# Kernel optimization log

Measured on AMD Instinct MI355X. Metric: run time of the kernel, lower is better.

Reference implementation:

```python
import jax, jax.numpy as jnp
import numpy as np
from jax import lax

V, E, H, B, S = 50257, 512, 1024, 128, 256

def setup_inputs() -> dict:
    key = jax.random.key(0)
    k0, k1, k2, k3, k4, k5 = jax.random.split(key, 6)
    scale = 1.0 / np.sqrt(H)  # PyTorch LSTMCell init range ~ U(-1/sqrt(H), 1/sqrt(H))
    return {
        "inputs": jax.random.randint(k0, (B, S), 0, V),
        "embed_table": jax.random.normal(k1, (V, E), dtype=jnp.float32) * 0.02,
        "W_ih": jax.random.uniform(k2, (4 * H, E), dtype=jnp.float32, minval=-scale, maxval=scale),
        "W_hh": jax.random.uniform(k3, (4 * H, H), dtype=jnp.float32, minval=-scale, maxval=scale),
        "b_ih": jax.random.uniform(k4, (4 * H,), dtype=jnp.float32, minval=-scale, maxval=scale),
        "b_hh": jax.random.uniform(k5, (4 * H,), dtype=jnp.float32, minval=-scale, maxval=scale),
    }

def reference(inputs, embed_table, W_ih, W_hh, b_ih, b_hh):
    # Embedding lookup: [B, S, E]
    embeds = embed_table[inputs]
    bias = b_ih + b_hh  # [4H]

    def step(h, x_t):
        # x_t: [B, E], h: [B, H]
        gates = x_t @ W_ih.T + h @ W_hh.T + bias  # [B, 4H]
        i, f, g, o = jnp.split(gates, 4, axis=-1)  # PyTorch gate order: i, f, g, o
        # FAITHFUL to original bug: new cell state is discarded each step, so the
        # carried cell state is always zero -> c_t = sigmoid(i) * tanh(g).
        c_t = jax.nn.sigmoid(i) * jnp.tanh(g)
        h_new = jax.nn.sigmoid(o) * jnp.tanh(c_t)
        return h_new, None

    h0 = jnp.zeros((B, H), dtype=embeds.dtype)
    xs = jnp.swapaxes(embeds, 0, 1)  # [S, B, E]
    h_last, _ = lax.scan(step, h0, xs)
    return h_last  # [B, H]
```

## Files before the change

kernel.cpp:

```cpp
#include <hip/hip_runtime.h>
#include <hip/hip_fp16.h>


typedef __fp16 f16x8 __attribute__((ext_vector_type(8)));
typedef __fp16 f16x4 __attribute__((ext_vector_type(4)));
typedef float  f32x4 __attribute__((ext_vector_type(4)));

#define MFMA16(a, b, c) __builtin_amdgcn_mfma_f32_16x16x32_f16(a, b, c, 0, 0, 0)

__device__ __forceinline__ float sigmoid_f(float x) {
  return 1.f / (1.f + __expf(-x));
}
__device__ __forceinline__ float tanh_f(float x) {
  x = fminf(fmaxf(x, -15.f), 15.f);
  float e = __expf(2.f * x);
  return (e - 1.f) / (e + 1.f);
}

static constexpr int SS = 256;

__global__ void prep_kernel(const float* __restrict__ W_ih, const float* __restrict__ W_hh,
                            const float* __restrict__ b_ih, const float* __restrict__ b_hh,
                            __fp16* __restrict__ Wi3, __fp16* __restrict__ Wh3,
                            float* __restrict__ bias3) {
  int j3 = blockIdx.x;
  int g = j3 >> 10, j = j3 & 1023;
  int orig = (g == 0 ? 0 : (g == 1 ? 2048 : 3072)) + j;
  int tid = threadIdx.x;
  {
    float4 v = *(const float4*)(W_hh + (size_t)orig * 1024 + tid * 4);
    f16x4 o = {(__fp16)v.x, (__fp16)v.y, (__fp16)v.z, (__fp16)v.w};
    *(f16x4*)(Wh3 + (size_t)j3 * 1024 + tid * 4) = o;
  }
  if (tid < 128) {
    float4 v = *(const float4*)(W_ih + (size_t)orig * 512 + tid * 4);
    f16x4 o = {(__fp16)v.x, (__fp16)v.y, (__fp16)v.z, (__fp16)v.w};
    *(f16x4*)(Wi3 + (size_t)j3 * 512 + tid * 4) = o;
  }
  if (tid == 0) bias3[j3] = b_ih[orig] + b_hh[orig];
}

__global__ void gather_kernel(const int* __restrict__ tok, const float* __restrict__ emb,
                              __fp16* __restrict__ X) {
  int m = blockIdx.x;
  int t = m >> 7, b = m & 127;
  int tk = tok[b * SS + t];
  int e0 = threadIdx.x * 8;
  const float* src = emb + (size_t)tk * 512 + e0;
  float4 v0 = *(const float4*)src;
  float4 v1 = *(const float4*)(src + 4);
  f16x8 o;
  o[0] = (__fp16)v0.x; o[1] = (__fp16)v0.y; o[2] = (__fp16)v0.z; o[3] = (__fp16)v0.w;
  o[4] = (__fp16)v1.x; o[5] = (__fp16)v1.y; o[6] = (__fp16)v1.z; o[7] = (__fp16)v1.w;
  *(f16x8*)(X + (size_t)m * 512 + e0) = o;
}

__global__ __launch_bounds__(512, 2) void recur_kernel(const __fp16* __restrict__ Wh3,
                                                       const __fp16* __restrict__ Wi3,
                                                       const __fp16* __restrict__ X,
                                                       const float* __restrict__ bias3,
                                                       __fp16* __restrict__ hbuf,
                                                       int* __restrict__ cnt,
                                                       float* __restrict__ out) {
  const int bid = blockIdx.x;
  const int bg = bid & 7, n = bid >> 3;
  const int b0 = bg * 16, j0 = n * 32;
  const int tid = threadIdx.x, wid = tid >> 6, lane = tid & 63;
  const int l15 = lane & 15, quad = lane >> 4;
  const int kq = wid >> 1, ct = wid & 1;
  const int ct_e = wid & 1, rq = wid >> 1;
  const int lr = lane >> 4;

  __shared__ float gbuf[2][4][3][2][16][20];

  f16x8 wh[3][8];
  f16x8 wi[3][4];
#pragma unroll
  for (int g = 0; g < 3; ++g) {
    const __fp16* wr = Wh3 + (size_t)(g * 1024 + j0 + ct * 16 + l15) * 1024 + kq * 256 + quad * 8;
#pragma unroll
    for (int kk = 0; kk < 8; ++kk) wh[g][kk] = *(const f16x8*)(wr + kk * 32);
    const __fp16* wr2 = Wi3 + (size_t)(g * 1024 + j0 + ct * 16 + l15) * 512 + kq * 128 + quad * 8;
#pragma unroll
    for (int kk = 0; kk < 4; ++kk) wi[g][kk] = *(const f16x8*)(wr2 + kk * 32);
  }

  float bs[3];
#pragma unroll
  for (int g = 0; g < 3; ++g) bs[g] = bias3[g * 1024 + j0 + ct_e * 16 + l15];

  const __fp16* xrow = X + (size_t)(b0 + l15) * 512 + kq * 128 + quad * 8;
  const __fp16* hrow = hbuf + (size_t)(b0 + l15) * 1024 + kq * 256 + quad * 8;
  int* cbase = cnt + bg * (SS * 16);

  f16x8 xa[4];
#pragma unroll
  for (int kk = 0; kk < 4; ++kk) xa[kk] = *(const f16x8*)(xrow + kk * 32);

  for (int t = 0; t < SS; ++t) {
    f32x4 acc[3];
#pragma unroll
    for (int g = 0; g < 3; ++g) {
      f32x4 z = {0.f, 0.f, 0.f, 0.f};
      acc[g] = z;
    }
#pragma unroll
    for (int kk = 0; kk < 4; ++kk)
#pragma unroll
      for (int g = 0; g < 3; ++g)
        acc[g] = MFMA16(xa[kk], wi[g][kk], acc[g]);
    {
      const int tn = (t + 1 < SS) ? t + 1 : t;
      const __fp16* xp = xrow + (size_t)tn * 65536;
#pragma unroll
      for (int kk = 0; kk < 4; ++kk) xa[kk] = *(const f16x8*)(xp + kk * 32);
    }
    if (t > 0) {
      const int* pollp = cbase + t * 16;
      for (;;) {
        int v = __hip_atomic_load(pollp, __ATOMIC_RELAXED, __HIP_MEMORY_SCOPE_AGENT);
        if (v >= 32) break;
        __builtin_amdgcn_s_sleep(1);
      }
      asm volatile("" ::: "memory");
    }
    f16x8 ha[8];
    {
      const __fp16* hp = hrow + (size_t)t * 131072;
#pragma unroll
      for (int kk = 0; kk < 8; ++kk) ha[kk] = *(const f16x8*)(hp + kk * 32);
    }
#pragma unroll
    for (int kk = 0; kk < 8; ++kk)
#pragma unroll
      for (int g = 0; g < 3; ++g)
        acc[g] = MFMA16(ha[kk], wh[g][kk], acc[g]);
    const int tp = t & 1;
#pragma unroll
    for (int g = 0; g < 3; ++g)
#pragma unroll
      for (int r = 0; r < 4; ++r)
        gbuf[tp][kq][g][ct][quad * 4 + r][l15] = acc[g][r];
    __syncthreads();
    {
      const int row_i = rq * 4 + lr;
      float s[3];
#pragma unroll
      for (int g = 0; g < 3; ++g)
        s[g] = gbuf[tp][0][g][ct_e][row_i][l15] + gbuf[tp][1][g][ct_e][row_i][l15] +
               gbuf[tp][2][g][ct_e][row_i][l15] + gbuf[tp][3][g][ct_e][row_i][l15];
      float gi = s[0] + bs[0];
      float gg = s[1] + bs[1];
      float go = s[2] + bs[2];
      float cv = sigmoid_f(gi) * tanh_f(gg);
      float hN = sigmoid_f(go) * tanh_f(cv);
      const int row = b0 + row_i;
      const int col = j0 + ct_e * 16 + l15;
      if (t == SS - 1) out[(size_t)row * 1024 + col] = hN;
      else hbuf[(size_t)(t + 1) * 131072 + (size_t)row * 1024 + col] = (__fp16)hN;
    }
    if (t < SS - 1) {
      asm volatile("s_waitcnt vmcnt(0)" ::: "memory");
      __syncthreads();
      if (tid == 0)
        __hip_atomic_fetch_add(cbase + (t + 1) * 16, 1,
                               __ATOMIC_RELAXED, __HIP_MEMORY_SCOPE_AGENT);
    }
  }
}

extern "C" void kernel_launch(void* const* d_in, const int* in_sizes, int n_in,
                              void* d_out, int out_size, void* d_ws, size_t ws_size,
                              hipStream_t stream) {
  const int*   tok  = (const int*)d_in[0];
  const float* emb  = (const float*)d_in[1];
  const float* W_ih = (const float*)d_in[2];
  const float* W_hh = (const float*)d_in[3];
  const float* b_ih = (const float*)d_in[4];
  const float* b_hh = (const float*)d_in[5];
  float* out = (float*)d_out;
  char* ws = (char*)d_ws;

  __fp16* X     = (__fp16*)(ws + 0);
  __fp16* Wi3   = (__fp16*)(ws + 33554432);
  __fp16* Wh3   = (__fp16*)(ws + 36700160);
  float*  bias3 = (float*) (ws + 42991616);
  int*    cnt   = (int*)   (ws + 43003904);
  __fp16* hbuf  = (__fp16*)(ws + 43134976);

  (void)hipMemsetAsync(cnt, 0, 131072, stream);
  (void)hipMemsetAsync(hbuf, 0, 131072 * 2, stream);

  prep_kernel<<<3072, 256, 0, stream>>>(W_ih, W_hh, b_ih, b_hh, Wi3, Wh3, bias3);
  gather_kernel<<<32768, 64, 0, stream>>>(tok, emb, X);
  recur_kernel<<<256, 512, 0, stream>>>(Wh3, Wi3, X, bias3, hbuf, cnt, out);
}
```

Baseline: 1.235 ms.

## Halve per-block column tile, launch 512 four-wave blocks, relax step barrier fencing

Each block now owns 16 hidden columns instead of 32 and runs 4 waves, so the grid grows to 512 blocks and the per-step arrival counter must reach 64. Each wave still holds its K-quarter of the weights in registers, and inline asm pins those weight registers. The explicit vmcnt wait and memory clobber around the step flag are removed. Instead, the h loads take a fake address dependency on the polled counter value (v>>8), which keeps them ordered after the poll. The intent is more parallelism and less per-step synchronisation latency. In exchange there are twice as many blocks signalling each counter, and the weaker ordering of hbuf stores before the release add risks memory-visibility races.

```diff
diff --git a/kernel.cpp b/kernel.cpp
--- a/kernel.cpp
+++ b/kernel.cpp
@@ -55,7 +55,7 @@
   *(f16x8*)(X + (size_t)m * 512 + e0) = o;
 }
 
-__global__ __launch_bounds__(512, 2) void recur_kernel(const __fp16* __restrict__ Wh3,
+__global__ __launch_bounds__(256, 2) void recur_kernel(const __fp16* __restrict__ Wh3,
                                                        const __fp16* __restrict__ Wi3,
                                                        const __fp16* __restrict__ X,
                                                        const float* __restrict__ bias3,
@@ -64,30 +64,35 @@
                                                        float* __restrict__ out) {
   const int bid = blockIdx.x;
   const int bg = bid & 7, n = bid >> 3;
-  const int b0 = bg * 16, j0 = n * 32;
+  const int b0 = bg * 16, j0 = n * 16;
   const int tid = threadIdx.x, wid = tid >> 6, lane = tid & 63;
   const int l15 = lane & 15, quad = lane >> 4;
-  const int kq = wid >> 1, ct = wid & 1;
-  const int ct_e = wid & 1, rq = wid >> 1;
-  const int lr = lane >> 4;
-
-  __shared__ float gbuf[2][4][3][2][16][20];
+  const int kq = wid;
+
+  __shared__ float gbuf[2][4][3][16][20];
 
   f16x8 wh[3][8];
   f16x8 wi[3][4];
 #pragma unroll
   for (int g = 0; g < 3; ++g) {
-    const __fp16* wr = Wh3 + (size_t)(g * 1024 + j0 + ct * 16 + l15) * 1024 + kq * 256 + quad * 8;
+    const __fp16* wr = Wh3 + (size_t)(g * 1024 + j0 + l15) * 1024 + kq * 256 + quad * 8;
 #pragma unroll
     for (int kk = 0; kk < 8; ++kk) wh[g][kk] = *(const f16x8*)(wr + kk * 32);
-    const __fp16* wr2 = Wi3 + (size_t)(g * 1024 + j0 + ct * 16 + l15) * 512 + kq * 128 + quad * 8;
+    const __fp16* wr2 = Wi3 + (size_t)(g * 1024 + j0 + l15) * 512 + kq * 128 + quad * 8;
 #pragma unroll
     for (int kk = 0; kk < 4; ++kk) wi[g][kk] = *(const f16x8*)(wr2 + kk * 32);
   }
+#pragma unroll
+  for (int g = 0; g < 3; ++g) {
+#pragma unroll
+    for (int kk = 0; kk < 8; ++kk) asm volatile("" : "+v"(wh[g][kk]));
+#pragma unroll
+    for (int kk = 0; kk < 4; ++kk) asm volatile("" : "+v"(wi[g][kk]));
+  }
 
   float bs[3];
 #pragma unroll
-  for (int g = 0; g < 3; ++g) bs[g] = bias3[g * 1024 + j0 + ct_e * 16 + l15];
+  for (int g = 0; g < 3; ++g) bs[g] = bias3[g * 1024 + j0 + l15];
 
   const __fp16* xrow = X + (size_t)(b0 + l15) * 512 + kq * 128 + quad * 8;
   const __fp16* hrow = hbuf + (size_t)(b0 + l15) * 1024 + kq * 256 + quad * 8;
@@ -115,18 +120,18 @@
 #pragma unroll
       for (int kk = 0; kk < 4; ++kk) xa[kk] = *(const f16x8*)(xp + kk * 32);
     }
+    int v = 64;
     if (t > 0) {
       const int* pollp = cbase + t * 16;
       for (;;) {
-        int v = __hip_atomic_load(pollp, __ATOMIC_RELAXED, __HIP_MEMORY_SCOPE_AGENT);
-        if (v >= 32) break;
+        v = __hip_atomic_load(pollp, __ATOMIC_RELAXED, __HIP_MEMORY_SCOPE_AGENT);
+        if (v >= 64) break;
         __builtin_amdgcn_s_sleep(1);
       }
-      asm volatile("" ::: "memory");
     }
     f16x8 ha[8];
     {
-      const __fp16* hp = hrow + (size_t)t * 131072;
+      const __fp16* hp = hrow + (size_t)t * 131072 + (v >> 8);
 #pragma unroll
       for (int kk = 0; kk < 8; ++kk) ha[kk] = *(const f16x8*)(hp + kk * 32);
     }
@@ -140,27 +145,26 @@
     for (int g = 0; g < 3; ++g)
 #pragma unroll
       for (int r = 0; r < 4; ++r)
-        gbuf[tp][kq][g][ct][quad * 4 + r][l15] = acc[g][r];
+        gbuf[tp][kq][g][quad * 4 + r][l15] = acc[g][r];
     __syncthreads();
     {
-      const int row_i = rq * 4 + lr;
+      const int row_i = kq * 4 + quad;
       float s[3];
 #pragma unroll
       for (int g = 0; g < 3; ++g)
-        s[g] = gbuf[tp][0][g][ct_e][row_i][l15] + gbuf[tp][1][g][ct_e][row_i][l15] +
-               gbuf[tp][2][g][ct_e][row_i][l15] + gbuf[tp][3][g][ct_e][row_i][l15];
+        s[g] = gbuf[tp][0][g][row_i][l15] + gbuf[tp][1][g][row_i][l15] +
+               gbuf[tp][2][g][row_i][l15] + gbuf[tp][3][g][row_i][l15];
       float gi = s[0] + bs[0];
       float gg = s[1] + bs[1];
       float go = s[2] + bs[2];
       float cv = sigmoid_f(gi) * tanh_f(gg);
       float hN = sigmoid_f(go) * tanh_f(cv);
       const int row = b0 + row_i;
-      const int col = j0 + ct_e * 16 + l15;
+      const int col = j0 + l15;
       if (t == SS - 1) out[(size_t)row * 1024 + col] = hN;
       else hbuf[(size_t)(t + 1) * 131072 + (size_t)row * 1024 + col] = (__fp16)hN;
     }
     if (t < SS - 1) {
-      asm volatile("s_waitcnt vmcnt(0)" ::: "memory");
       __syncthreads();
       if (tid == 0)
         __hip_atomic_fetch_add(cbase + (t + 1) * 16, 1,
@@ -193,5 +197,5 @@
 
   prep_kernel<<<3072, 256, 0, stream>>>(W_ih, W_hh, b_ih, b_hh, Wi3, Wh3, bias3);
   gather_kernel<<<32768, 64, 0, stream>>>(tok, emb, X);
-  recur_kernel<<<256, 512, 0, stream>>>(Wh3, Wi3, X, bias3, hbuf, cnt, out);
-}
+  recur_kernel<<<512, 256, 0, stream>>>(Wh3, Wi3, X, bias3, hbuf, cnt, out);
+}
```

New measurement: 2.109 ms. 1.71x slower.

## Halve recurrent block to 4 waves with 2-way K split and per-wave signaling

Applied to the files above, without the earlier changes.

Changes the recurrent kernel from 8 waves with a 4-way K split to 4 waves with a 2-way K split. Each wave now holds twice as many weight registers. The cross-wave reduction becomes a single LDS handoff from half the waves, and the post-step __syncthreads is removed in favour of per-wave atomic increments, with the poll threshold raised to 64. The aim is to shorten the per-timestep critical path by cutting LDS reduction and barrier work. The cost is much higher register pressure (wh[3][16] plus ha[16] per lane), more serial MFMA per wave, and more atomic traffic. Sigmoid and tanh also switch to a hardware reciprocal instead of division.

```diff
diff --git a/kernel.cpp b/kernel.cpp
--- a/kernel.cpp
+++ b/kernel.cpp
@@ -8,13 +8,14 @@
 
 #define MFMA16(a, b, c) __builtin_amdgcn_mfma_f32_16x16x32_f16(a, b, c, 0, 0, 0)
 
+__device__ __forceinline__ float rcp_f(float x) { return __builtin_amdgcn_rcpf(x); }
 __device__ __forceinline__ float sigmoid_f(float x) {
-  return 1.f / (1.f + __expf(-x));
+  return rcp_f(1.f + __expf(-x));
 }
 __device__ __forceinline__ float tanh_f(float x) {
   x = fminf(fmaxf(x, -15.f), 15.f);
   float e = __expf(2.f * x);
-  return (e - 1.f) / (e + 1.f);
+  return 1.f - 2.f * rcp_f(e + 1.f);
 }
 
 static constexpr int SS = 256;
@@ -55,7 +56,7 @@
   *(f16x8*)(X + (size_t)m * 512 + e0) = o;
 }
 
-__global__ __launch_bounds__(512, 2) void recur_kernel(const __fp16* __restrict__ Wh3,
+__global__ __launch_bounds__(256, 1) void recur_kernel(const __fp16* __restrict__ Wh3,
                                                        const __fp16* __restrict__ Wi3,
                                                        const __fp16* __restrict__ X,
                                                        const float* __restrict__ bias3,
@@ -67,35 +68,34 @@
   const int b0 = bg * 16, j0 = n * 32;
   const int tid = threadIdx.x, wid = tid >> 6, lane = tid & 63;
   const int l15 = lane & 15, quad = lane >> 4;
-  const int kq = wid >> 1, ct = wid & 1;
-  const int ct_e = wid & 1, rq = wid >> 1;
-  const int lr = lane >> 4;
+  const int tile = wid & 1, kh = wid >> 1;
+  const int col = j0 + tile * 16 + l15;
 
-  __shared__ float gbuf[2][4][3][2][16][20];
+  __shared__ float gbuf[2][2][3][16][20];
 
-  f16x8 wh[3][8];
-  f16x8 wi[3][4];
+  f16x8 wi[3][8];
+  f16x8 wh[3][16];
 #pragma unroll
   for (int g = 0; g < 3; ++g) {
-    const __fp16* wr = Wh3 + (size_t)(g * 1024 + j0 + ct * 16 + l15) * 1024 + kq * 256 + quad * 8;
+    const __fp16* wr2 = Wi3 + (size_t)(g * 1024 + col) * 512 + kh * 256 + quad * 8;
 #pragma unroll
-    for (int kk = 0; kk < 8; ++kk) wh[g][kk] = *(const f16x8*)(wr + kk * 32);
-    const __fp16* wr2 = Wi3 + (size_t)(g * 1024 + j0 + ct * 16 + l15) * 512 + kq * 128 + quad * 8;
+    for (int kk = 0; kk < 8; ++kk) wi[g][kk] = *(const f16x8*)(wr2 + kk * 32);
+    const __fp16* wr = Wh3 + (size_t)(g * 1024 + col) * 1024 + kh * 512 + quad * 8;
 #pragma unroll
-    for (int kk = 0; kk < 4; ++kk) wi[g][kk] = *(const f16x8*)(wr2 + kk * 32);
+    for (int kk = 0; kk < 16; ++kk) wh[g][kk] = *(const f16x8*)(wr + kk * 32);
   }
 
   float bs[3];
 #pragma unroll
-  for (int g = 0; g < 3; ++g) bs[g] = bias3[g * 1024 + j0 + ct_e * 16 + l15];
+  for (int g = 0; g < 3; ++g) bs[g] = bias3[g * 1024 + col];
 
-  const __fp16* xrow = X + (size_t)(b0 + l15) * 512 + kq * 128 + quad * 8;
-  const __fp16* hrow = hbuf + (size_t)(b0 + l15) * 1024 + kq * 256 + quad * 8;
+  const __fp16* xrow = X + (size_t)(b0 + l15) * 512 + kh * 256 + quad * 8;
+  const __fp16* hrow = hbuf + (size_t)(b0 + l15) * 1024 + kh * 512 + quad * 8;
   int* cbase = cnt + bg * (SS * 16);
 
-  f16x8 xa[4];
+  f16x8 xa[8];
 #pragma unroll
-  for (int kk = 0; kk < 4; ++kk) xa[kk] = *(const f16x8*)(xrow + kk * 32);
+  for (int kk = 0; kk < 8; ++kk) xa[kk] = *(const f16x8*)(xrow + kk * 32);
 
   for (int t = 0; t < SS; ++t) {
     f32x4 acc[3];
@@ -105,7 +105,7 @@
       acc[g] = z;
     }
 #pragma unroll
-    for (int kk = 0; kk < 4; ++kk)
+    for (int kk = 0; kk < 8; ++kk)
 #pragma unroll
       for (int g = 0; g < 3; ++g)
         acc[g] = MFMA16(xa[kk], wi[g][kk], acc[g]);
@@ -113,58 +113,56 @@
       const int tn = (t + 1 < SS) ? t + 1 : t;
       const __fp16* xp = xrow + (size_t)tn * 65536;
 #pragma unroll
-      for (int kk = 0; kk < 4; ++kk) xa[kk] = *(const f16x8*)(xp + kk * 32);
+      for (int kk = 0; kk < 8; ++kk) xa[kk] = *(const f16x8*)(xp + kk * 32);
     }
     if (t > 0) {
       const int* pollp = cbase + t * 16;
       for (;;) {
         int v = __hip_atomic_load(pollp, __ATOMIC_RELAXED, __HIP_MEMORY_SCOPE_AGENT);
-        if (v >= 32) break;
+        if (v >= 64) break;
         __builtin_amdgcn_s_sleep(1);
       }
       asm volatile("" ::: "memory");
     }
-    f16x8 ha[8];
+    f16x8 ha[16];
     {
       const __fp16* hp = hrow + (size_t)t * 131072;
 #pragma unroll
-      for (int kk = 0; kk < 8; ++kk) ha[kk] = *(const f16x8*)(hp + kk * 32);
+      for (int kk = 0; kk < 16; ++kk) ha[kk] = *(const f16x8*)(hp + kk * 32);
     }
 #pragma unroll
-    for (int kk = 0; kk < 8; ++kk)
+    for (int kk = 0; kk < 16; ++kk)
 #pragma unroll
       for (int g = 0; g < 3; ++g)
         acc[g] = MFMA16(ha[kk], wh[g][kk], acc[g]);
     const int tp = t & 1;
-#pragma unroll
-    for (int g = 0; g < 3; ++g)
-#pragma unroll
-      for (int r = 0; r < 4; ++r)
-        gbuf[tp][kq][g][ct][quad * 4 + r][l15] = acc[g][r];
-    __syncthreads();
-    {
-      const int row_i = rq * 4 + lr;
-      float s[3];
+    if (kh == 0) {
 #pragma unroll
       for (int g = 0; g < 3; ++g)
-        s[g] = gbuf[tp][0][g][ct_e][row_i][l15] + gbuf[tp][1][g][ct_e][row_i][l15] +
-               gbuf[tp][2][g][ct_e][row_i][l15] + gbuf[tp][3][g][ct_e][row_i][l15];
-      float gi = s[0] + bs[0];
-      float gg = s[1] + bs[1];
-      float go = s[2] + bs[2];
-      float cv = sigmoid_f(gi) * tanh_f(gg);
-      float hN = sigmoid_f(go) * tanh_f(cv);
-      const int row = b0 + row_i;
-      const int col = j0 + ct_e * 16 + l15;
-      if (t == SS - 1) out[(size_t)row * 1024 + col] = hN;
-      else hbuf[(size_t)(t + 1) * 131072 + (size_t)row * 1024 + col] = (__fp16)hN;
+#pragma unroll
+        for (int r = 0; r < 4; ++r)
+          gbuf[tp][tile][g][quad * 4 + r][l15] = acc[g][r];
     }
-    if (t < SS - 1) {
-      asm volatile("s_waitcnt vmcnt(0)" ::: "memory");
-      __syncthreads();
-      if (tid == 0)
-        __hip_atomic_fetch_add(cbase + (t + 1) * 16, 1,
-                               __ATOMIC_RELAXED, __HIP_MEMORY_SCOPE_AGENT);
+    __syncthreads();
+    if (kh == 1) {
+#pragma unroll
+      for (int r = 0; r < 4; ++r) {
+        const int row_i = quad * 4 + r;
+        float gi = acc[0][r] + gbuf[tp][tile][0][row_i][l15] + bs[0];
+        float gg = acc[1][r] + gbuf[tp][tile][1][row_i][l15] + bs[1];
+        float go = acc[2][r] + gbuf[tp][tile][2][row_i][l15] + bs[2];
+        float cv = sigmoid_f(gi) * tanh_f(gg);
+        float hN = sigmoid_f(go) * tanh_f(cv);
+        const int row = b0 + row_i;
+        if (t == SS - 1) out[(size_t)row * 1024 + col] = hN;
+        else hbuf[(size_t)(t + 1) * 131072 + (size_t)row * 1024 + col] = (__fp16)hN;
+      }
+      if (t < SS - 1) {
+        asm volatile("s_waitcnt vmcnt(0)" ::: "memory");
+        if (lane == 0)
+          __hip_atomic_fetch_add(cbase + (t + 1) * 16, 1,
+                                 __ATOMIC_RELAXED, __HIP_MEMORY_SCOPE_AGENT);
+      }
     }
   }
 }
@@ -193,5 +191,5 @@
 
   prep_kernel<<<3072, 256, 0, stream>>>(W_ih, W_hh, b_ih, b_hh, Wi3, Wh3, bias3);
   gather_kernel<<<32768, 64, 0, stream>>>(tok, emb, X);
-  recur_kernel<<<256, 512, 0, stream>>>(Wh3, Wi3, X, bias3, hbuf, cnt, out);
+  recur_kernel<<<256, 256, 0, stream>>>(Wh3, Wi3, X, bias3, hbuf, cnt, out);
 }
```

Measured after the change: 1.786 ms. +44.7%, slower.
